# Kernel optimization log

Measured on AMD Instinct MI355X. Metric: run time of the kernel, lower is better.

Reference implementation:

```python
import jax, jax.numpy as jnp
import numpy as np

B_SZ = 512; S = 3; F = 5; C = 62; E = 5
D_MODEL = C * E * F          # 1550
N_LAYERS = 2
D_STATE = 16
EXPAND = 2
D_CONV = 4
ED = EXPAND * D_MODEL        # 3100
DT_RANK = (D_MODEL + 15) // 16  # 97
VOCAB = 128
EPS = 1e-5


def setup_inputs() -> dict:
    key = jax.random.key(0)
    ks = jax.random.split(key, 10)
    def g(i, shape, scale=0.02):
        return jax.random.normal(ks[i], shape, dtype=jnp.float32) * scale
    A_log = jnp.tile(jnp.log(jnp.arange(1, D_STATE + 1, dtype=jnp.float32))[None, None, :],
                     (N_LAYERS, ED, 1))
    return {
        "x": jax.random.normal(ks[0], (B_SZ, S, F, C, E), dtype=jnp.float32),
        "in_proj_w": g(1, (N_LAYERS, 2 * ED, D_MODEL)),
        "conv_w": g(2, (N_LAYERS, ED, 1, D_CONV), 0.1),
        "conv_b": jnp.zeros((N_LAYERS, ED), jnp.float32),
        "x_proj_w": g(3, (N_LAYERS, DT_RANK + 2 * D_STATE, ED)),
        "dt_proj_w": g(4, (N_LAYERS, ED, DT_RANK), 0.1),
        "dt_proj_b": jnp.full((N_LAYERS, ED), -4.6, jnp.float32),  # softplus ~ 0.01
        "A_log": A_log,
        "D_param": jnp.ones((N_LAYERS, ED), jnp.float32),
        "out_proj_w": g(5, (N_LAYERS, D_MODEL, ED)),
        "norm_w": jnp.ones((N_LAYERS, D_MODEL), jnp.float32),
        "normf_w": jnp.ones((D_MODEL,), jnp.float32),
        "lm_head_w": g(6, (VOCAB, D_MODEL)),
        "bn_w": jnp.ones((F,), jnp.float32),
        "bn_b": jnp.zeros((F,), jnp.float32),
        "emb_w": g(7, (256, VOCAB)),
        "emb_b": jnp.zeros((256,), jnp.float32),
    }


def _rmsnorm(x, w):
    return x * jax.lax.rsqrt(jnp.mean(x * x, axis=-1, keepdims=True) + EPS) * w


def _silu(x):
    return x * jax.nn.sigmoid(x)


def _causal_conv(xt, w, b):
    # xt: (B, ED, L); w: (ED, 1, K) depthwise causal conv (pad K-1 left)
    y = jax.lax.conv_general_dilated(xt, w, (1,), [(D_CONV - 1, 0)],
                                     feature_group_count=ED)
    return y + b[None, :, None]


def _ssm_scan(deltaA, deltaBx, Cm):
    # deltaA, deltaBx: (B, L, ED, N); Cm: (B, L, N)
    def step(h, inp):
        dA, dBx, c = inp
        h = dA * h + dBx                      # (B, ED, N)
        y = jnp.einsum('ben,bn->be', h, c)    # (B, ED)
        return h, y
    h0 = jnp.zeros((deltaA.shape[0], ED, D_STATE), deltaA.dtype)
    xs = (deltaA.transpose(1, 0, 2, 3), deltaBx.transpose(1, 0, 2, 3), Cm.transpose(1, 0, 2))
    _, ys = jax.lax.scan(step, h0, xs)
    return ys.transpose(1, 0, 2)              # (B, L, ED)


def _mixer(h, in_w, cw, cb, xp_w, dt_w, dt_b, A_log, Dp, out_w):
    # h: (B, L, D_MODEL)
    xz = jnp.einsum('bld,ed->ble', h, in_w)   # (B, L, 2*ED)
    x_in, z = jnp.split(xz, 2, axis=-1)
    xc = _silu(_causal_conv(x_in.transpose(0, 2, 1), cw, cb).transpose(0, 2, 1))  # (B,L,ED)
    dbc = jnp.einsum('ble,re->blr', xc, xp_w)  # (B, L, DT_RANK + 2N)
    dt = dbc[..., :DT_RANK]
    Bm = dbc[..., DT_RANK:DT_RANK + D_STATE]
    Cm = dbc[..., DT_RANK + D_STATE:]
    delta = jax.nn.softplus(jnp.einsum('blr,er->ble', dt, dt_w) + dt_b)  # (B,L,ED)
    A = -jnp.exp(A_log)                       # (ED, N)
    deltaA = jnp.exp(delta[..., None] * A)                       # (B,L,ED,N)
    deltaBx = delta[..., None] * Bm[:, :, None, :] * xc[..., None]
    y = _ssm_scan(deltaA, deltaBx, Cm) + Dp * xc
    return jnp.einsum('ble,de->bld', y * _silu(z), out_w)


def reference(x, in_proj_w, conv_w, conv_b, x_proj_w, dt_proj_w, dt_proj_b,
              A_log, D_param, out_proj_w, norm_w, normf_w, lm_head_w,
              bn_w, bn_b, emb_w, emb_b):
    b, s, f, c, e = x.shape
    fx = x.transpose(0, 1, 3, 2, 4).reshape(b, s, c * f * e)  # (B, S, D_MODEL)
    h = fx
    for l in range(N_LAYERS):
        h = h + _mixer(_rmsnorm(h, norm_w[l]), in_proj_w[l], conv_w[l], conv_b[l],
                       x_proj_w[l], dt_proj_w[l], dt_proj_b[l], A_log[l],
                       D_param[l], out_proj_w[l])
    h = _rmsnorm(h, normf_w)
    logits = jnp.einsum('bsd,vd->bsv', h, lm_head_w)          # (B, S, 128)
    m = jnp.broadcast_to(logits[:, None], (b, f, s, VOCAB))    # repeat over f
    # BatchNorm2d(feature_dim) in training mode: stats over (B, S, VOCAB) per channel f
    mean = jnp.mean(m, axis=(0, 2, 3), keepdims=True)
    var = jnp.var(m, axis=(0, 2, 3), keepdims=True)
    mn = (m - mean) * jax.lax.rsqrt(var + EPS)
    mn = mn * bn_w[None, :, None, None] + bn_b[None, :, None, None]
    return jnp.einsum('bfsv,ov->bfso', mn, emb_w) + emb_b      # (B, F, S, 256)
```

## Files before the change

kernel.cpp:

```cpp
#include <hip/hip_runtime.h>
#include <hip/hip_bf16.h>
#include <math.h>

#define B_SZ 512
#define SEQ 3
#define D_MODEL 1550
#define ED 3100
#define NSTATE 16
#define DTR 97
#define DBC_R 129
#define VOCAB 128
#define NBS (B_SZ*SEQ)
#define EPSV 1e-5f

#define KD 1600
#define KE 3136
#define NIP 6272
#define NXP 256
#define NOP 1664
#define NDT 3200
#define KDT 128
#define DBC_LD 256

#define QIP 2508800
#define QXP 200704
#define QDT 102400
#define QOP 1304576
#define AEL 49600
#define QLM 51200
#define TEL 32768
#define PREP_N1 4166080
#define PREP_N0 4250306

static inline int cdiv_h(int a, int b){ return (a + b - 1) / b; }

__device__ __forceinline__ float silu_f(float x){ return x / (1.0f + expf(-x)); }

using bf16x8 = __attribute__((ext_vector_type(8))) short;
using f32x4  = __attribute__((ext_vector_type(4))) float;

__device__ __forceinline__ void gload16(const void* g, void* l){
  __builtin_amdgcn_global_load_lds(
      (const __attribute__((address_space(1))) unsigned int*)g,
      (__attribute__((address_space(3))) unsigned int*)l,
      16, 0, 0);
}

__device__ __forceinline__ unsigned short bfbits(float v){
  __hip_bfloat16 b = __float2bfloat16(v);
  return *(unsigned short*)&b;
}

__global__ __launch_bounds__(256)
void k_perm_rms(const float* __restrict__ x, const float* __restrict__ w,
                float* __restrict__ h, __hip_bfloat16* __restrict__ hn){
  int row = blockIdx.x;
  const float* xr = x + (size_t)row * D_MODEL;
  float vreg[7]; int dreg[7];
  int cnt = 0;
  float ss = 0.f;
  for (int i = threadIdx.x; i < D_MODEL; i += 256){
    float v = xr[i];
    int e = i % 5, c = (i / 5) % 62, f = i / 310;
    int d = (c * 5 + f) * 5 + e;
    vreg[cnt] = v; dreg[cnt] = d; cnt++;
    ss = fmaf(v, v, ss);
    h[(size_t)row * D_MODEL + d] = v;
  }
  __shared__ float red[4];
  __shared__ float sscale;
  int lane = threadIdx.x & 63, wv = threadIdx.x >> 6;
  #pragma unroll
  for (int o = 32; o > 0; o >>= 1) ss += __shfl_down(ss, o, 64);
  if (lane == 0) red[wv] = ss;
  __syncthreads();
  if (threadIdx.x == 0){
    float t = red[0] + red[1] + red[2] + red[3];
    sscale = 1.0f / sqrtf(t / (float)D_MODEL + EPSV);
  }
  __syncthreads();
  float sc = sscale;
  __hip_bfloat16* orow = hn + (size_t)row * KD;
  for (int k = 0; k < cnt; k++)
    orow[dreg[k]] = __float2bfloat16(vreg[k] * sc * w[dreg[k]]);
  for (int i = D_MODEL + threadIdx.x; i < KD; i += 256)
    orow[i] = __float2bfloat16(0.f);
}

__global__ __launch_bounds__(256)
void k_rms_res(float* __restrict__ h, const __hip_bfloat16* __restrict__ part,
               const float* __restrict__ w, __hip_bfloat16* __restrict__ hn){
  int row = blockIdx.x;
  size_t hb = (size_t)row * D_MODEL;
  float vreg[7];
  int cnt = 0;
  float ss = 0.f;
  for (int i = threadIdx.x; i < D_MODEL; i += 256){
    float v = h[hb + i];
    #pragma unroll
    for (int p = 0; p < 4; p++)
      v += __bfloat162float(part[(size_t)p * NBS * D_MODEL + hb + i]);
    h[hb + i] = v;
    vreg[cnt++] = v;
    ss = fmaf(v, v, ss);
  }
  __shared__ float red[4];
  __shared__ float sscale;
  int lane = threadIdx.x & 63, wv = threadIdx.x >> 6;
  #pragma unroll
  for (int o = 32; o > 0; o >>= 1) ss += __shfl_down(ss, o, 64);
  if (lane == 0) red[wv] = ss;
  __syncthreads();
  if (threadIdx.x == 0){
    float t = red[0] + red[1] + red[2] + red[3];
    sscale = 1.0f / sqrtf(t / (float)D_MODEL + EPSV);
  }
  __syncthreads();
  float sc = sscale;
  __hip_bfloat16* orow = hn + (size_t)row * KD;
  for (int k = 0; k < cnt; k++){
    int i = threadIdx.x + k * 256;
    orow[i] = __float2bfloat16(vreg[k] * sc * w[i]);
  }
  for (int i = D_MODEL + threadIdx.x; i < KD; i += 256)
    orow[i] = __float2bfloat16(0.f);
}

__device__ __forceinline__ void cast4(const float* __restrict__ src,
                                      __hip_bfloat16* __restrict__ dst,
                                      int q, int N, int K, int Kp){
  int i4 = q * 4;
  int row = i4 / Kp;
  int col = i4 % Kp;
  const float* srow = src + (size_t)row * K;
  ushort4 o;
  o.x = bfbits((row < N && col + 0 < K) ? srow[col + 0] : 0.f);
  o.y = bfbits((row < N && col + 1 < K) ? srow[col + 1] : 0.f);
  o.z = bfbits((row < N && col + 2 < K) ? srow[col + 2] : 0.f);
  o.w = bfbits((row < N && col + 3 < K) ? srow[col + 3] : 0.f);
  *(ushort4*)(dst + i4) = o;
}

__global__ __launch_bounds__(256)
void k_prep(const float* __restrict__ ipw, const float* __restrict__ xpw,
            const float* __restrict__ dtw, const float* __restrict__ opw,
            const float* __restrict__ alog,
            const float* __restrict__ lmw, const float* __restrict__ embw,
            __hip_bfloat16* __restrict__ ipb, __hip_bfloat16* __restrict__ xpb,
            __hip_bfloat16* __restrict__ dtwb, __hip_bfloat16* __restrict__ opb,
            float* __restrict__ A_t,
            __hip_bfloat16* __restrict__ lmb,
            float* __restrict__ emb_t, float* __restrict__ sumw,
            float* __restrict__ stats, int l0){
  int idx = blockIdx.x * 256 + threadIdx.x;
  if (idx < QIP){ cast4(ipw, ipb, idx, 2 * ED, D_MODEL, KD); return; } idx -= QIP;
  if (idx < QXP){ cast4(xpw, xpb, idx, DBC_R, ED, KE); return; } idx -= QXP;
  if (idx < QDT){ cast4(dtw, dtwb, idx, ED, DTR, KDT); return; } idx -= QDT;
  if (idx < QOP){ cast4(opw, opb, idx, D_MODEL, ED, KE); return; } idx -= QOP;
  if (idx < AEL){
    int n = idx / ED, ch = idx % ED;
    A_t[idx] = -expf(alog[(size_t)ch * NSTATE + n]);
    return;
  } idx -= AEL;
  if (!l0) return;
  if (idx < QLM){ cast4(lmw, lmb, idx, VOCAB, D_MODEL, KD); return; } idx -= QLM;
  if (idx < TEL){
    int v = idx >> 8, o = idx & 255;
    emb_t[idx] = embw[(size_t)o * VOCAB + v];
    return;
  } idx -= TEL;
  if (idx < 256){
    const float* r = embw + (size_t)idx * VOCAB;
    float s = 0.f;
    for (int v = 0; v < VOCAB; v++) s += r[v];
    sumw[idx] = s;
    return;
  } idx -= 256;
  if (idx < 2) stats[idx] = 0.f;
}

template<int SPLITS, bool OUT_BF16, bool PARTIAL>
__global__ __launch_bounds__(256)
void k_gemm3(const __hip_bfloat16* __restrict__ A, const __hip_bfloat16* __restrict__ B,
             void* Cv, int Kp, int Nld, int Nreal){
  __shared__ short Al[3][4096];
  __shared__ short Bl[3][4096];
  const int gx = gridDim.x, gy = gridDim.y;
  const int nwg = gx * gy;
  const int wg = blockIdx.y * gx + blockIdx.x;
  const int q = nwg >> 3, r = nwg & 7;
  const int xcd = wg & 7, off = wg >> 3;
  const int nid = (xcd < r ? xcd * (q + 1) : r * (q + 1) + (xcd - r) * q) + off;
  const int bm = (nid % gy) * 128;
  const int bn = (nid / gy) * 128;

  const int t = threadIdx.x;
  const int tt8 = t * 8;

  int kb = 0, ke = Kp;
  if (SPLITS > 1){
    int Kc = ((Kp / SPLITS + 31) / 32) * 32;
    kb = blockIdx.z * Kc;
    ke = min(kb + Kc, Kp);
    if (kb >= ke) return;
  }
  const int nt = (ke - kb) / 32;

  const int cg = ((t & 3) ^ ((t >> 2) & 3)) * 8;
  const short* Ab = (const short*)A;
  const short* Bb = (const short*)B;
  const short* ga0 = Ab + (size_t)(bm + (t >> 2)) * Kp + cg;
  const short* ga1 = Ab + (size_t)(bm + 64 + (t >> 2)) * Kp + cg;
  const short* gb0 = Bb + (size_t)(bn + (t >> 2)) * Kp + cg;
  const short* gb1 = Bb + (size_t)(bn + 64 + (t >> 2)) * Kp + cg;

  const int l = t & 63;
  const int wid = t >> 6;
  const int wr = wid >> 1, wc = wid & 1;
  const int fr = l & 15;
  const int cc = ((l >> 4) ^ (l & 3)) * 8;

  f32x4 acc[4][4] = {};

#define STAGE(buf, kof) do{ \
    gload16(ga0 + (kof), &Al[buf][tt8]); \
    gload16(ga1 + (kof), &Al[buf][2048 + tt8]); \
    gload16(gb0 + (kof), &Bl[buf][tt8]); \
    gload16(gb1 + (kof), &Bl[buf][2048 + tt8]); }while(0)

  STAGE(0, kb);
  if (nt > 1) STAGE(1, kb + 32);
  int bsel = 0, snext = 2;
  for (int it = 0; it < nt; ++it){
    if (it + 1 < nt) asm volatile("s_waitcnt vmcnt(4)" ::: "memory");
    else             asm volatile("s_waitcnt vmcnt(0)" ::: "memory");
    __builtin_amdgcn_s_barrier();
    asm volatile("" ::: "memory");
    __builtin_amdgcn_sched_barrier(0);
    if (it + 2 < nt) STAGE(snext, kb + (it + 2) * 32);
    bf16x8 af[4], bfr[4];
    #pragma unroll
    for (int m = 0; m < 4; m++)
      af[m] = *(const bf16x8*)&Al[bsel][(wr * 64 + m * 16 + fr) * 32 + cc];
    #pragma unroll
    for (int n = 0; n < 4; n++)
      bfr[n] = *(const bf16x8*)&Bl[bsel][(wc * 64 + n * 16 + fr) * 32 + cc];
    #pragma unroll
    for (int m = 0; m < 4; m++)
      #pragma unroll
      for (int n = 0; n < 4; n++)
        acc[m][n] = __builtin_amdgcn_mfma_f32_16x16x32_bf16(af[m], bfr[n], acc[m][n], 0, 0, 0);
    bsel = (bsel == 2) ? 0 : bsel + 1;
    snext = (snext == 2) ? 0 : snext + 1;
  }
#undef STAGE

  float* Cf = (float*)Cv;
  __hip_bfloat16* Cb = (__hip_bfloat16*)Cv;
  if (PARTIAL){
    const size_t pstride = (size_t)gy * 128 * Nld;
    if (OUT_BF16) Cb += (size_t)blockIdx.z * pstride;
    else          Cf += (size_t)blockIdx.z * pstride;
  }
  const int r0 = (l >> 4) * 4;
  #pragma unroll
  for (int m = 0; m < 4; m++){
    #pragma unroll
    for (int n = 0; n < 4; n++){
      int col = bn + wc * 64 + n * 16 + fr;
      if (col < Nreal){
        size_t base = (size_t)(bm + wr * 64 + m * 16 + r0) * Nld + col;
        #pragma unroll
        for (int j = 0; j < 4; j++){
          float v = acc[m][n][j];
          size_t o = base + (size_t)j * Nld;
          if (OUT_BF16) Cb[o] = __float2bfloat16(v);
          else          Cf[o] = v;
        }
      }
    }
  }
}

__global__ void k_conv_silu(const __hip_bfloat16* __restrict__ xz, const float* __restrict__ cw,
                            const float* __restrict__ cb, __hip_bfloat16* __restrict__ xc_b){
  int idx = blockIdx.x * 256 + threadIdx.x;
  if (idx >= B_SZ * KE) return;
  int ch = idx % KE;
  int b  = idx / KE;
  size_t ob = (size_t)b * SEQ * KE + ch;
  if (ch >= ED){
    __hip_bfloat16 z = __float2bfloat16(0.f);
    xc_b[ob] = z; xc_b[ob + KE] = z; xc_b[ob + 2 * KE] = z;
    return;
  }
  const __hip_bfloat16* base = xz + (size_t)b * SEQ * NIP + ch;
  float x0 = __bfloat162float(base[0]);
  float x1 = __bfloat162float(base[NIP]);
  float x2 = __bfloat162float(base[2 * NIP]);
  const float* w = cw + (size_t)ch * 4;
  float w1 = w[1], w2 = w[2], w3 = w[3];
  float bb = cb[ch];
  float s0 = silu_f(fmaf(w3, x0, bb));
  float s1 = silu_f(fmaf(w2, x0, fmaf(w3, x1, bb)));
  float s2 = silu_f(fmaf(w1, x0, fmaf(w2, x1, fmaf(w3, x2, bb))));
  xc_b[ob]          = __float2bfloat16(s0);
  xc_b[ob + KE]     = __float2bfloat16(s1);
  xc_b[ob + 2 * KE] = __float2bfloat16(s2);
}

__global__ __launch_bounds__(256)
void k_xred(const float* __restrict__ part, float* __restrict__ dbc,
            __hip_bfloat16* __restrict__ dbc_b){
  int idx = blockIdx.x * 256 + threadIdx.x;
  if (idx >= NBS * DBC_LD) return;
  float s = 0.f;
  #pragma unroll
  for (int p = 0; p < 8; p++) s += part[(size_t)p * NBS * DBC_LD + idx];
  dbc[idx] = s;
  int c = idx & 255, row = idx >> 8;
  if (c < KDT) dbc_b[(size_t)row * KDT + c] = __float2bfloat16(c < DTR ? s : 0.f);
}

__global__ __launch_bounds__(256)
void k_scan2(const __hip_bfloat16* __restrict__ delta_b, const float* __restrict__ dbc,
             const float* __restrict__ dtb, const float* __restrict__ A_t,
             const float* __restrict__ Dp, const __hip_bfloat16* __restrict__ xz,
             __hip_bfloat16* __restrict__ xc_b){
  __shared__ float sB[SEQ][NSTATE], sC[SEQ][NSTATE];
  int b = blockIdx.y;
  if (threadIdx.x < SEQ * 2 * NSTATE){
    int t = threadIdx.x / (2 * NSTATE), r = threadIdx.x % (2 * NSTATE);
    float v = dbc[(size_t)(b * SEQ + t) * DBC_LD + DTR + r];
    if (r < NSTATE) sB[t][r] = v; else sC[t][r - NSTATE] = v;
  }
  __syncthreads();
  int ch = blockIdx.x * 256 + threadIdx.x;
  if (ch >= ED) return;

  float bias = dtb[ch];
  float dlt[SEQ];
  #pragma unroll
  for (int t = 0; t < SEQ; t++){
    float acc = __bfloat162float(delta_b[(size_t)(b * SEQ + t) * NDT + ch]) + bias;
    dlt[t] = (acc > 20.f) ? acc : log1pf(expf(acc));
  }

  size_t ob = (size_t)b * SEQ * KE + ch;
  float xcv[SEQ] = { __bfloat162float(xc_b[ob]),
                     __bfloat162float(xc_b[ob + KE]),
                     __bfloat162float(xc_b[ob + 2 * KE]) };
  float y[SEQ] = {0.f, 0.f, 0.f};
  #pragma unroll
  for (int n = 0; n < NSTATE; n++){
    float Av = A_t[(size_t)n * ED + ch];
    float hs = 0.f;
    #pragma unroll
    for (int t = 0; t < SEQ; t++){
      float dA = expf(dlt[t] * Av);
      hs = fmaf(dA, hs, dlt[t] * sB[t][n] * xcv[t]);
      y[t] = fmaf(hs, sC[t][n], y[t]);
    }
  }
  float dp = Dp[ch];
  const __hip_bfloat16* zbase = xz + (size_t)b * SEQ * NIP + ED + ch;
  #pragma unroll
  for (int t = 0; t < SEQ; t++){
    float z = __bfloat162float(zbase[(size_t)t * NIP]);
    float yy = fmaf(dp, xcv[t], y[t]);
    xc_b[ob + (size_t)t * KE] = __float2bfloat16(yy * silu_f(z));
  }
}

__global__ __launch_bounds__(256)
void k_statsred(const float* __restrict__ part, float* __restrict__ logits,
                float* __restrict__ stats){
  float s = 0.f, ss = 0.f;
  for (int i = blockIdx.x * 256 + threadIdx.x; i < NBS * VOCAB; i += gridDim.x * 256){
    float v = 0.f;
    #pragma unroll
    for (int p = 0; p < 4; p++) v += part[(size_t)p * NBS * VOCAB + i];
    logits[i] = v;
    s += v; ss = fmaf(v, v, ss);
  }
  #pragma unroll
  for (int o = 32; o > 0; o >>= 1){ s += __shfl_down(s, o, 64); ss += __shfl_down(ss, o, 64); }
  __shared__ float rs[4], rss[4];
  int lane = threadIdx.x & 63, wv = threadIdx.x >> 6;
  if (lane == 0){ rs[wv] = s; rss[wv] = ss; }
  __syncthreads();
  if (threadIdx.x == 0){
    atomicAdd(&stats[0], rs[0] + rs[1] + rs[2] + rs[3]);
    atomicAdd(&stats[1], rss[0] + rss[1] + rss[2] + rss[3]);
  }
}

__global__ __launch_bounds__(256)
void k_projfinal(const float* __restrict__ logits, const float* __restrict__ emb_t,
                 const float* __restrict__ sumw, const float* __restrict__ stats,
                 const float* __restrict__ bnw, const float* __restrict__ bnb,
                 const float* __restrict__ embb, float* __restrict__ out){
  __shared__ float row[VOCAB];
  int r = blockIdx.x;
  int o = threadIdx.x;
  if (o < VOCAB) row[o] = logits[(size_t)r * VOCAB + o];
  __syncthreads();
  float p = 0.f;
  #pragma unroll 8
  for (int v = 0; v < VOCAB; v++) p = fmaf(row[v], emb_t[v * 256 + o], p);
  const float invN = 1.0f / (float)(NBS * VOCAB);
  float mean = stats[0] * invN;
  float var  = stats[1] * invN - mean * mean;
  float rstd = rsqrtf(var + EPSV);
  int b = r / SEQ, s = r % SEQ;
  float sw = sumw[o];
  float base = rstd * (p - mean * sw);
  float eb = embb[o];
  #pragma unroll
  for (int f = 0; f < 5; f++){
    out[(((size_t)(b * 5 + f)) * SEQ + s) * 256 + o] = bnw[f] * base + bnb[f] * sw + eb;
  }
}

extern "C" void kernel_launch(void* const* d_in, const int* in_sizes, int n_in,
                              void* d_out, int out_size, void* d_ws, size_t ws_size,
                              hipStream_t stream) {
  const float* x          = (const float*)d_in[0];
  const float* in_proj_w  = (const float*)d_in[1];
  const float* conv_w     = (const float*)d_in[2];
  const float* conv_b     = (const float*)d_in[3];
  const float* x_proj_w   = (const float*)d_in[4];
  const float* dt_proj_w  = (const float*)d_in[5];
  const float* dt_proj_b  = (const float*)d_in[6];
  const float* A_log      = (const float*)d_in[7];
  const float* D_param    = (const float*)d_in[8];
  const float* out_proj_w = (const float*)d_in[9];
  const float* norm_w     = (const float*)d_in[10];
  const float* normf_w    = (const float*)d_in[11];
  const float* lm_head_w  = (const float*)d_in[12];
  const float* bn_w       = (const float*)d_in[13];
  const float* bn_b       = (const float*)d_in[14];
  const float* emb_w      = (const float*)d_in[15];
  const float* emb_b      = (const float*)d_in[16];

  float* ws = (float*)d_ws;
  float* h      = ws;
  float* dbc    = h      + (size_t)NBS * D_MODEL;
  float* logits = dbc    + (size_t)NBS * DBC_LD;
  float* sumw   = logits + (size_t)NBS * VOCAB;
  float* stats  = sumw   + 256;
  float* A_t    = stats  + 2;
  float* emb_t  = A_t    + (size_t)NSTATE * ED;
  float* spart  = emb_t  + (size_t)VOCAB * 256;
  size_t spart_f = ((size_t)4 * NBS * D_MODEL * 2 + 3) / 4;
  float* xpart  = spart;
  float* lmpart = spart;
  __hip_bfloat16* opart = (__hip_bfloat16*)spart;
  __hip_bfloat16* xz_b   = (__hip_bfloat16*)(spart + spart_f);
  __hip_bfloat16* hn_b   = xz_b   + (size_t)NBS * NIP;
  __hip_bfloat16* xc_b   = hn_b   + (size_t)NBS * KD;
  __hip_bfloat16* dbc_b  = xc_b   + (size_t)NBS * KE;
  __hip_bfloat16* dlt_b  = dbc_b  + (size_t)NBS * KDT;
  __hip_bfloat16* ipb    = dlt_b  + (size_t)NBS * NDT;
  __hip_bfloat16* xpb    = ipb    + (size_t)NIP * KD;
  __hip_bfloat16* dtwb   = xpb    + (size_t)NXP * KE;
  __hip_bfloat16* opb    = dtwb   + (size_t)NDT * KDT;
  __hip_bfloat16* lmb    = opb    + (size_t)NOP * KE;
  size_t need = (size_t)((char*)(lmb + (size_t)VOCAB * KD) - (char*)ws);
  if (ws_size < need) return;

  for (int l = 0; l < 2; l++){
    const float* ipw = in_proj_w  + (size_t)l * 2 * ED * D_MODEL;
    const float* cw  = conv_w     + (size_t)l * ED * 4;
    const float* cb  = conv_b     + (size_t)l * ED;
    const float* xpw = x_proj_w   + (size_t)l * DBC_R * ED;
    const float* dtw = dt_proj_w  + (size_t)l * ED * DTR;
    const float* dtb = dt_proj_b  + (size_t)l * ED;
    const float* al  = A_log      + (size_t)l * ED * NSTATE;
    const float* dp  = D_param    + (size_t)l * ED;
    const float* opw = out_proj_w + (size_t)l * D_MODEL * ED;
    const float* nw  = norm_w     + (size_t)l * D_MODEL;

    k_prep<<<cdiv_h(l == 0 ? PREP_N0 : PREP_N1, 256), 256, 0, stream>>>(
        ipw, xpw, dtw, opw, al, lm_head_w, emb_w,
        ipb, xpb, dtwb, opb, A_t, lmb, emb_t, sumw, stats, l == 0 ? 1 : 0);

    if (l == 0){
      k_perm_rms<<<NBS, 256, 0, stream>>>(x, nw, h, hn_b);
    } else {
      k_rms_res<<<NBS, 256, 0, stream>>>(h, opart, nw, hn_b);
    }

    k_gemm3<1, true, false><<<dim3(NIP / 128, NBS / 128, 1), 256, 0, stream>>>(
        hn_b, ipb, xz_b, KD, NIP, NIP);

    k_conv_silu<<<cdiv_h(B_SZ * KE, 256), 256, 0, stream>>>(xz_b, cw, cb, xc_b);

    k_gemm3<8, false, true><<<dim3(NXP / 128, NBS / 128, 8), 256, 0, stream>>>(
        xc_b, xpb, xpart, KE, DBC_LD, DBC_LD);
    k_xred<<<cdiv_h(NBS * DBC_LD, 256), 256, 0, stream>>>(xpart, dbc, dbc_b);

    k_gemm3<1, true, false><<<dim3(NDT / 128, NBS / 128, 1), 256, 0, stream>>>(
        dbc_b, dtwb, dlt_b, KDT, NDT, NDT);

    k_scan2<<<dim3(cdiv_h(ED, 256), B_SZ), 256, 0, stream>>>(
        dlt_b, dbc, dtb, A_t, dp, xz_b, xc_b);

    k_gemm3<4, true, true><<<dim3(NOP / 128, NBS / 128, 4), 256, 0, stream>>>(
        xc_b, opb, opart, KE, D_MODEL, D_MODEL);
  }

  k_rms_res<<<NBS, 256, 0, stream>>>(h, opart, normf_w, hn_b);
  k_gemm3<4, false, true><<<dim3(1, NBS / 128, 4), 256, 0, stream>>>(
      hn_b, lmb, lmpart, KD, VOCAB, VOCAB);
  k_statsred<<<192, 256, 0, stream>>>(lmpart, logits, stats);

  k_projfinal<<<NBS, 256, 0, stream>>>(logits, emb_t, sumw, stats,
                                       bn_w, bn_b, emb_b, (float*)d_out);
}
```

Before: 480.6 us.

## Fuse RMSNorm into prep kernel and vectorize conv, xred, and scan kernels

Merges the per-layer RMSNorm (perm/residual variant) into the weight-cast prep kernel by appending NBS extra blocks, saving one launch per layer. Vectorizes k_conv_silu to four channels per thread, k_xred to float4 loads, and k_scan2 to two channels per thread with paired loads. The aim is to cut launch overhead and the number of memory transactions in the elementwise kernels. The cost is higher register use, and the vector loads depend on the alignment guaranteed by padded strides.

```diff
diff --git a/kernel.cpp b/kernel.cpp
--- a/kernel.cpp
+++ b/kernel.cpp
@@ -31,6 +31,8 @@
 #define TEL 32768
 #define PREP_N1 4166080
 #define PREP_N0 4250306
+#define PB_N1 16274
+#define PB_N0 16603
 
 static inline int cdiv_h(int a, int b){ return (a + b - 1) / b; }
 
@@ -50,80 +52,9 @@
   __hip_bfloat16 b = __float2bfloat16(v);
   return *(unsigned short*)&b;
 }
-
-__global__ __launch_bounds__(256)
-void k_perm_rms(const float* __restrict__ x, const float* __restrict__ w,
-                float* __restrict__ h, __hip_bfloat16* __restrict__ hn){
-  int row = blockIdx.x;
-  const float* xr = x + (size_t)row * D_MODEL;
-  float vreg[7]; int dreg[7];
-  int cnt = 0;
-  float ss = 0.f;
-  for (int i = threadIdx.x; i < D_MODEL; i += 256){
-    float v = xr[i];
-    int e = i % 5, c = (i / 5) % 62, f = i / 310;
-    int d = (c * 5 + f) * 5 + e;
-    vreg[cnt] = v; dreg[cnt] = d; cnt++;
-    ss = fmaf(v, v, ss);
-    h[(size_t)row * D_MODEL + d] = v;
-  }
-  __shared__ float red[4];
-  __shared__ float sscale;
-  int lane = threadIdx.x & 63, wv = threadIdx.x >> 6;
-  #pragma unroll
-  for (int o = 32; o > 0; o >>= 1) ss += __shfl_down(ss, o, 64);
-  if (lane == 0) red[wv] = ss;
-  __syncthreads();
-  if (threadIdx.x == 0){
-    float t = red[0] + red[1] + red[2] + red[3];
-    sscale = 1.0f / sqrtf(t / (float)D_MODEL + EPSV);
-  }
-  __syncthreads();
-  float sc = sscale;
-  __hip_bfloat16* orow = hn + (size_t)row * KD;
-  for (int k = 0; k < cnt; k++)
-    orow[dreg[k]] = __float2bfloat16(vreg[k] * sc * w[dreg[k]]);
-  for (int i = D_MODEL + threadIdx.x; i < KD; i += 256)
-    orow[i] = __float2bfloat16(0.f);
-}
-
-__global__ __launch_bounds__(256)
-void k_rms_res(float* __restrict__ h, const __hip_bfloat16* __restrict__ part,
-               const float* __restrict__ w, __hip_bfloat16* __restrict__ hn){
-  int row = blockIdx.x;
-  size_t hb = (size_t)row * D_MODEL;
-  float vreg[7];
-  int cnt = 0;
-  float ss = 0.f;
-  for (int i = threadIdx.x; i < D_MODEL; i += 256){
-    float v = h[hb + i];
-    #pragma unroll
-    for (int p = 0; p < 4; p++)
-      v += __bfloat162float(part[(size_t)p * NBS * D_MODEL + hb + i]);
-    h[hb + i] = v;
-    vreg[cnt++] = v;
-    ss = fmaf(v, v, ss);
-  }
-  __shared__ float red[4];
-  __shared__ float sscale;
-  int lane = threadIdx.x & 63, wv = threadIdx.x >> 6;
-  #pragma unroll
-  for (int o = 32; o > 0; o >>= 1) ss += __shfl_down(ss, o, 64);
-  if (lane == 0) red[wv] = ss;
-  __syncthreads();
-  if (threadIdx.x == 0){
-    float t = red[0] + red[1] + red[2] + red[3];
-    sscale = 1.0f / sqrtf(t / (float)D_MODEL + EPSV);
-  }
-  __syncthreads();
-  float sc = sscale;
-  __hip_bfloat16* orow = hn + (size_t)row * KD;
-  for (int k = 0; k < cnt; k++){
-    int i = threadIdx.x + k * 256;
-    orow[i] = __float2bfloat16(vreg[k] * sc * w[i]);
-  }
-  for (int i = D_MODEL + threadIdx.x; i < KD; i += 256)
-    orow[i] = __float2bfloat16(0.f);
+__device__ __forceinline__ float bf2f(unsigned short u){
+  unsigned int x = ((unsigned int)u) << 16;
+  return *(float*)&x;
 }
 
 __device__ __forceinline__ void cast4(const float* __restrict__ src,
@@ -141,6 +72,62 @@
   *(ushort4*)(dst + i4) = o;
 }
 
+__device__ void rms_body(int row, int mode,
+                         const float* __restrict__ x,
+                         const __hip_bfloat16* __restrict__ part,
+                         float* __restrict__ h, const float* __restrict__ w,
+                         __hip_bfloat16* __restrict__ hn){
+  float vreg[7]; int dreg[7];
+  int cnt = 0;
+  float ss = 0.f;
+  if (mode == 0){
+    const float* xr = x + (size_t)row * D_MODEL;
+    for (int i = threadIdx.x; i < D_MODEL; i += 256){
+      float v = xr[i];
+      int e = i % 5, c = (i / 5) % 62, f = i / 310;
+      int d = (c * 5 + f) * 5 + e;
+      vreg[cnt] = v; dreg[cnt] = d; cnt++;
+      ss = fmaf(v, v, ss);
+      h[(size_t)row * D_MODEL + d] = v;
+    }
+  } else {
+    size_t hb = (size_t)row * D_MODEL;
+    for (int i = threadIdx.x; i < D_MODEL; i += 256){
+      float v = h[hb + i];
+      #pragma unroll
+      for (int p = 0; p < 4; p++)
+        v += __bfloat162float(part[(size_t)p * NBS * D_MODEL + hb + i]);
+      h[hb + i] = v;
+      vreg[cnt] = v; dreg[cnt] = i; cnt++;
+      ss = fmaf(v, v, ss);
+    }
+  }
+  __shared__ float red[4];
+  __shared__ float sscale;
+  int lane = threadIdx.x & 63, wv = threadIdx.x >> 6;
+  #pragma unroll
+  for (int o = 32; o > 0; o >>= 1) ss += __shfl_down(ss, o, 64);
+  if (lane == 0) red[wv] = ss;
+  __syncthreads();
+  if (threadIdx.x == 0){
+    float t = red[0] + red[1] + red[2] + red[3];
+    sscale = 1.0f / sqrtf(t / (float)D_MODEL + EPSV);
+  }
+  __syncthreads();
+  float sc = sscale;
+  __hip_bfloat16* orow = hn + (size_t)row * KD;
+  for (int k = 0; k < cnt; k++)
+    orow[dreg[k]] = __float2bfloat16(vreg[k] * sc * w[dreg[k]]);
+  for (int i = D_MODEL + threadIdx.x; i < KD; i += 256)
+    orow[i] = __float2bfloat16(0.f);
+}
+
+__global__ __launch_bounds__(256)
+void k_rms_res(float* __restrict__ h, const __hip_bfloat16* __restrict__ part,
+               const float* __restrict__ w, __hip_bfloat16* __restrict__ hn){
+  rms_body(blockIdx.x, 1, nullptr, part, h, w, hn);
+}
+
 __global__ __launch_bounds__(256)
 void k_prep(const float* __restrict__ ipw, const float* __restrict__ xpw,
             const float* __restrict__ dtw, const float* __restrict__ opw,
@@ -151,7 +138,14 @@
             float* __restrict__ A_t,
             __hip_bfloat16* __restrict__ lmb,
             float* __restrict__ emb_t, float* __restrict__ sumw,
-            float* __restrict__ stats, int l0){
+            float* __restrict__ stats, int l0, int castBlocks,
+            const float* __restrict__ x, const __hip_bfloat16* __restrict__ part,
+            float* __restrict__ h, const float* __restrict__ nw,
+            __hip_bfloat16* __restrict__ hn){
+  if ((int)blockIdx.x >= castBlocks){
+    rms_body(blockIdx.x - castBlocks, l0 ? 0 : 1, x, part, h, nw, hn);
+    return;
+  }
   int idx = blockIdx.x * 256 + threadIdx.x;
   if (idx < QIP){ cast4(ipw, ipb, idx, 2 * ED, D_MODEL, KD); return; } idx -= QIP;
   if (idx < QXP){ cast4(xpw, xpb, idx, DBC_R, ED, KE); return; } idx -= QXP;
@@ -282,44 +276,69 @@
   }
 }
 
-__global__ void k_conv_silu(const __hip_bfloat16* __restrict__ xz, const float* __restrict__ cw,
-                            const float* __restrict__ cb, __hip_bfloat16* __restrict__ xc_b){
+__global__ __launch_bounds__(256)
+void k_conv_silu(const __hip_bfloat16* __restrict__ xz, const float* __restrict__ cw,
+                 const float* __restrict__ cb, __hip_bfloat16* __restrict__ xc_b){
   int idx = blockIdx.x * 256 + threadIdx.x;
-  if (idx >= B_SZ * KE) return;
-  int ch = idx % KE;
-  int b  = idx / KE;
+  if (idx >= B_SZ * (KE / 4)) return;
+  int ch = (idx % (KE / 4)) * 4;
+  int b  = idx / (KE / 4);
   size_t ob = (size_t)b * SEQ * KE + ch;
   if (ch >= ED){
-    __hip_bfloat16 z = __float2bfloat16(0.f);
-    xc_b[ob] = z; xc_b[ob + KE] = z; xc_b[ob + 2 * KE] = z;
+    ushort4 z = {0, 0, 0, 0};
+    *(ushort4*)&xc_b[ob] = z;
+    *(ushort4*)&xc_b[ob + KE] = z;
+    *(ushort4*)&xc_b[ob + 2 * KE] = z;
     return;
   }
-  const __hip_bfloat16* base = xz + (size_t)b * SEQ * NIP + ch;
-  float x0 = __bfloat162float(base[0]);
-  float x1 = __bfloat162float(base[NIP]);
-  float x2 = __bfloat162float(base[2 * NIP]);
-  const float* w = cw + (size_t)ch * 4;
-  float w1 = w[1], w2 = w[2], w3 = w[3];
-  float bb = cb[ch];
-  float s0 = silu_f(fmaf(w3, x0, bb));
-  float s1 = silu_f(fmaf(w2, x0, fmaf(w3, x1, bb)));
-  float s2 = silu_f(fmaf(w1, x0, fmaf(w2, x1, fmaf(w3, x2, bb))));
-  xc_b[ob]          = __float2bfloat16(s0);
-  xc_b[ob + KE]     = __float2bfloat16(s1);
-  xc_b[ob + 2 * KE] = __float2bfloat16(s2);
+  size_t rb = (size_t)b * SEQ * NIP + ch;
+  ushort4 u0 = *(const ushort4*)&xz[rb];
+  ushort4 u1 = *(const ushort4*)&xz[rb + NIP];
+  ushort4 u2 = *(const ushort4*)&xz[rb + 2 * NIP];
+  float4 cbv = *(const float4*)&cb[ch];
+  ushort4 o0, o1, o2;
+  #pragma unroll
+  for (int j = 0; j < 4; j++){
+    float x0 = bf2f(j == 0 ? u0.x : j == 1 ? u0.y : j == 2 ? u0.z : u0.w);
+    float x1 = bf2f(j == 0 ? u1.x : j == 1 ? u1.y : j == 2 ? u1.z : u1.w);
+    float x2 = bf2f(j == 0 ? u2.x : j == 1 ? u2.y : j == 2 ? u2.z : u2.w);
+    float4 w = *(const float4*)&cw[(size_t)(ch + j) * 4];
+    float bb = j == 0 ? cbv.x : j == 1 ? cbv.y : j == 2 ? cbv.z : cbv.w;
+    unsigned short s0 = bfbits(silu_f(fmaf(w.w, x0, bb)));
+    unsigned short s1 = bfbits(silu_f(fmaf(w.z, x0, fmaf(w.w, x1, bb))));
+    unsigned short s2 = bfbits(silu_f(fmaf(w.y, x0, fmaf(w.z, x1, fmaf(w.w, x2, bb)))));
+    if (j == 0){ o0.x = s0; o1.x = s1; o2.x = s2; }
+    else if (j == 1){ o0.y = s0; o1.y = s1; o2.y = s2; }
+    else if (j == 2){ o0.z = s0; o1.z = s1; o2.z = s2; }
+    else { o0.w = s0; o1.w = s1; o2.w = s2; }
+  }
+  *(ushort4*)&xc_b[ob]          = o0;
+  *(ushort4*)&xc_b[ob + KE]     = o1;
+  *(ushort4*)&xc_b[ob + 2 * KE] = o2;
 }
 
 __global__ __launch_bounds__(256)
 void k_xred(const float* __restrict__ part, float* __restrict__ dbc,
             __hip_bfloat16* __restrict__ dbc_b){
-  int idx = blockIdx.x * 256 + threadIdx.x;
-  if (idx >= NBS * DBC_LD) return;
-  float s = 0.f;
-  #pragma unroll
-  for (int p = 0; p < 8; p++) s += part[(size_t)p * NBS * DBC_LD + idx];
-  dbc[idx] = s;
-  int c = idx & 255, row = idx >> 8;
-  if (c < KDT) dbc_b[(size_t)row * KDT + c] = __float2bfloat16(c < DTR ? s : 0.f);
+  int q = blockIdx.x * 256 + threadIdx.x;
+  if (q >= NBS * DBC_LD / 4) return;
+  int i4 = q * 4;
+  float4 s = {0.f, 0.f, 0.f, 0.f};
+  #pragma unroll
+  for (int p = 0; p < 8; p++){
+    float4 v = *(const float4*)&part[(size_t)p * NBS * DBC_LD + i4];
+    s.x += v.x; s.y += v.y; s.z += v.z; s.w += v.w;
+  }
+  *(float4*)&dbc[i4] = s;
+  int c = i4 & 255, row = i4 >> 8;
+  if (c < KDT){
+    ushort4 o;
+    o.x = bfbits(c + 0 < DTR ? s.x : 0.f);
+    o.y = bfbits(c + 1 < DTR ? s.y : 0.f);
+    o.z = bfbits(c + 2 < DTR ? s.z : 0.f);
+    o.w = bfbits(c + 3 < DTR ? s.w : 0.f);
+    *(ushort4*)&dbc_b[(size_t)row * KDT + c] = o;
+  }
 }
 
 __global__ __launch_bounds__(256)
@@ -335,40 +354,52 @@
     if (r < NSTATE) sB[t][r] = v; else sC[t][r - NSTATE] = v;
   }
   __syncthreads();
-  int ch = blockIdx.x * 256 + threadIdx.x;
+  int ch = (blockIdx.x * 256 + threadIdx.x) * 2;
   if (ch >= ED) return;
 
-  float bias = dtb[ch];
-  float dlt[SEQ];
+  float2 bias = *(const float2*)&dtb[ch];
+  float dlt[2][SEQ];
   #pragma unroll
   for (int t = 0; t < SEQ; t++){
-    float acc = __bfloat162float(delta_b[(size_t)(b * SEQ + t) * NDT + ch]) + bias;
-    dlt[t] = (acc > 20.f) ? acc : log1pf(expf(acc));
+    ushort2 u = *(const ushort2*)&delta_b[(size_t)(b * SEQ + t) * NDT + ch];
+    float a0 = bf2f(u.x) + bias.x;
+    float a1 = bf2f(u.y) + bias.y;
+    dlt[0][t] = (a0 > 20.f) ? a0 : log1pf(expf(a0));
+    dlt[1][t] = (a1 > 20.f) ? a1 : log1pf(expf(a1));
   }
 
   size_t ob = (size_t)b * SEQ * KE + ch;
-  float xcv[SEQ] = { __bfloat162float(xc_b[ob]),
-                     __bfloat162float(xc_b[ob + KE]),
-                     __bfloat162float(xc_b[ob + 2 * KE]) };
-  float y[SEQ] = {0.f, 0.f, 0.f};
+  float xcv[2][SEQ];
+  #pragma unroll
+  for (int t = 0; t < SEQ; t++){
+    ushort2 u = *(const ushort2*)&xc_b[ob + (size_t)t * KE];
+    xcv[0][t] = bf2f(u.x); xcv[1][t] = bf2f(u.y);
+  }
+  float y[2][SEQ] = {};
   #pragma unroll
   for (int n = 0; n < NSTATE; n++){
-    float Av = A_t[(size_t)n * ED + ch];
-    float hs = 0.f;
+    float2 Av = *(const float2*)&A_t[(size_t)n * ED + ch];
+    float hs0 = 0.f, hs1 = 0.f;
     #pragma unroll
     for (int t = 0; t < SEQ; t++){
-      float dA = expf(dlt[t] * Av);
-      hs = fmaf(dA, hs, dlt[t] * sB[t][n] * xcv[t]);
-      y[t] = fmaf(hs, sC[t][n], y[t]);
+      float Bn = sB[t][n], Cn = sC[t][n];
+      float dA0 = expf(dlt[0][t] * Av.x);
+      float dA1 = expf(dlt[1][t] * Av.y);
+      hs0 = fmaf(dA0, hs0, dlt[0][t] * Bn * xcv[0][t]);
+      hs1 = fmaf(dA1, hs1, dlt[1][t] * Bn * xcv[1][t]);
+      y[0][t] = fmaf(hs0, Cn, y[0][t]);
+      y[1][t] = fmaf(hs1, Cn, y[1][t]);
     }
   }
-  float dp = Dp[ch];
+  float2 dp = *(const float2*)&Dp[ch];
   const __hip_bfloat16* zbase = xz + (size_t)b * SEQ * NIP + ED + ch;
   #pragma unroll
   for (int t = 0; t < SEQ; t++){
-    float z = __bfloat162float(zbase[(size_t)t * NIP]);
-    float yy = fmaf(dp, xcv[t], y[t]);
-    xc_b[ob + (size_t)t * KE] = __float2bfloat16(yy * silu_f(z));
+    ushort2 uz = *(const ushort2*)&zbase[(size_t)t * NIP];
+    float y0 = fmaf(dp.x, xcv[0][t], y[0][t]) * silu_f(bf2f(uz.x));
+    float y1 = fmaf(dp.y, xcv[1][t], y[1][t]) * silu_f(bf2f(uz.y));
+    ushort2 o; o.x = bfbits(y0); o.y = bfbits(y1);
+    *(ushort2*)&xc_b[ob + (size_t)t * KE] = o;
   }
 }
 
@@ -481,29 +512,25 @@
     const float* opw = out_proj_w + (size_t)l * D_MODEL * ED;
     const float* nw  = norm_w     + (size_t)l * D_MODEL;
 
-    k_prep<<<cdiv_h(l == 0 ? PREP_N0 : PREP_N1, 256), 256, 0, stream>>>(
+    int cblk = (l == 0) ? PB_N0 : PB_N1;
+    k_prep<<<cblk + NBS, 256, 0, stream>>>(
         ipw, xpw, dtw, opw, al, lm_head_w, emb_w,
-        ipb, xpb, dtwb, opb, A_t, lmb, emb_t, sumw, stats, l == 0 ? 1 : 0);
-
-    if (l == 0){
-      k_perm_rms<<<NBS, 256, 0, stream>>>(x, nw, h, hn_b);
-    } else {
-      k_rms_res<<<NBS, 256, 0, stream>>>(h, opart, nw, hn_b);
-    }
+        ipb, xpb, dtwb, opb, A_t, lmb, emb_t, sumw, stats, l == 0 ? 1 : 0,
+        cblk, x, opart, h, nw, hn_b);
 
     k_gemm3<1, true, false><<<dim3(NIP / 128, NBS / 128, 1), 256, 0, stream>>>(
         hn_b, ipb, xz_b, KD, NIP, NIP);
 
-    k_conv_silu<<<cdiv_h(B_SZ * KE, 256), 256, 0, stream>>>(xz_b, cw, cb, xc_b);
+    k_conv_silu<<<cdiv_h(B_SZ * (KE / 4), 256), 256, 0, stream>>>(xz_b, cw, cb, xc_b);
 
     k_gemm3<8, false, true><<<dim3(NXP / 128, NBS / 128, 8), 256, 0, stream>>>(
         xc_b, xpb, xpart, KE, DBC_LD, DBC_LD);
-    k_xred<<<cdiv_h(NBS * DBC_LD, 256), 256, 0, stream>>>(xpart, dbc, dbc_b);
+    k_xred<<<cdiv_h(NBS * DBC_LD / 4, 256), 256, 0, stream>>>(xpart, dbc, dbc_b);
 
     k_gemm3<1, true, false><<<dim3(NDT / 128, NBS / 128, 1), 256, 0, stream>>>(
         dbc_b, dtwb, dlt_b, KDT, NDT, NDT);
 
-    k_scan2<<<dim3(cdiv_h(ED, 256), B_SZ), 256, 0, stream>>>(
+    k_scan2<<<dim3(cdiv_h(ED / 2, 256), B_SZ), 256, 0, stream>>>(
         dlt_b, dbc, dtb, A_t, dp, xz_b, xc_b);
 
     k_gemm3<4, true, true><<<dim3(NOP / 128, NBS / 128, 4), 256, 0, stream>>>(
```

Result: slower. 491.7 us (+2.3%).
